# Optimization experiments

Hardware: AMD Instinct MI355X
Metric: run time of the kernel (lower is better)

Reference implementation:

```python
import jax, jax.numpy as jnp
import numpy as np


def setup_inputs() -> dict:
    key = jax.random.key(0)
    k1, k2, k3, k4 = jax.random.split(key, 4)
    B, S, K, N = 2, 1024, 4096, 4096
    x = jax.random.normal(k1, (B, S, K), dtype=jnp.float32)
    # int8 weights in [-128, 127]
    weight = jax.random.randint(k2, (N, K), -128, 128, dtype=jnp.int8)
    # per-output-channel dequant scales (small positive values)
    scales = jax.random.uniform(k3, (N,), dtype=jnp.float32, minval=0.005, maxval=0.02)
    bias = jax.random.normal(k4, (N,), dtype=jnp.float32) * 0.1
    return {"x": x, "weight": weight, "scales": scales, "bias": bias}


def reference(x, weight, scales, bias):
    # F.linear(x, weight.to(x.dtype)): [B,S,K] @ [N,K]^T -> [B,S,N]
    w = weight.astype(x.dtype)
    y = jnp.einsum('bsk,nk->bsn', x, w)
    # per-output-channel scale + bias epilogue
    return y * scales + bias
```

## Files before the change

### kernel.cpp

```cpp
#include <hip/hip_runtime.h>
#include <hip/hip_bf16.h>
#include <stdint.h>

#define M_DIM 2048
#define N_DIM 4096
#define K_DIM 4096

#define BM 128
#define BN 256
#define BK 128

#define NSLOT 3
#define ASLOT (BM * BK)
#define BSLOT (BN * BK)

#define NT (K_DIM / BK)

typedef __attribute__((ext_vector_type(4))) int   int4v;
typedef __attribute__((ext_vector_type(4))) float f32x4;

__device__ __forceinline__ void load_lds16(const void* g, void* l) {
    __builtin_amdgcn_global_load_lds(
        (const __attribute__((address_space(1))) void*)g,
        (__attribute__((address_space(3))) void*)l,
        16, 0, 0);
}

__global__ __launch_bounds__(256) void quant_x(const float* __restrict__ x,
                                               int8_t* __restrict__ Aq,
                                               float* __restrict__ sx) {
    const int row = blockIdx.x;
    const int tid = threadIdx.x;
    const float4* xr = (const float4*)(x + (size_t)row * K_DIM);

    float4 v[4];
    float mx = 0.f;
#pragma unroll
    for (int p = 0; p < 4; p++) {
        v[p] = xr[p * 256 + tid];
        mx = fmaxf(mx, fmaxf(fmaxf(fabsf(v[p].x), fabsf(v[p].y)),
                             fmaxf(fabsf(v[p].z), fabsf(v[p].w))));
    }
#pragma unroll
    for (int off = 32; off >= 1; off >>= 1)
        mx = fmaxf(mx, __shfl_xor(mx, off, 64));

    __shared__ float wmax[4];
    __shared__ float smax;
    if ((tid & 63) == 0) wmax[tid >> 6] = mx;
    __syncthreads();
    if (tid == 0) {
        float m = fmaxf(fmaxf(wmax[0], wmax[1]), fmaxf(wmax[2], wmax[3]));
        m = fmaxf(m, 1e-20f);
        smax = m;
        sx[row] = m * (1.0f / 127.0f);
    }
    __syncthreads();
    const float inv = 127.0f / smax;

    int* out = (int*)Aq + (size_t)row * (K_DIM / 4);
#pragma unroll
    for (int p = 0; p < 4; p++) {
        int q0 = (int)__builtin_rintf(v[p].x * inv);
        int q1 = (int)__builtin_rintf(v[p].y * inv);
        int q2 = (int)__builtin_rintf(v[p].z * inv);
        int q3 = (int)__builtin_rintf(v[p].w * inv);
        q0 = max(-127, min(127, q0)); q1 = max(-127, min(127, q1));
        q2 = max(-127, min(127, q2)); q3 = max(-127, min(127, q3));
        out[p * 256 + tid] = (q0 & 255) | ((q1 & 255) << 8) |
                             ((q2 & 255) << 16) | ((q3 & 255) << 24);
    }
}

__global__ __launch_bounds__(256) void cvt_w8(const int* __restrict__ w,
                                              int8_t* __restrict__ Bq) {
    size_t i = ((size_t)blockIdx.x * 256 + threadIdx.x) * 16;
    int4 a0 = *(const int4*)(w + i);
    int4 a1 = *(const int4*)(w + i + 4);
    int4 a2 = *(const int4*)(w + i + 8);
    int4 a3 = *(const int4*)(w + i + 12);
    uint4 t;
    t.x = (a0.x & 255) | ((a0.y & 255) << 8) | ((a0.z & 255) << 16) | ((a0.w & 255) << 24);
    t.y = (a1.x & 255) | ((a1.y & 255) << 8) | ((a1.z & 255) << 16) | ((a1.w & 255) << 24);
    t.z = (a2.x & 255) | ((a2.y & 255) << 8) | ((a2.z & 255) << 16) | ((a2.w & 255) << 24);
    t.w = (a3.x & 255) | ((a3.y & 255) << 8) | ((a3.z & 255) << 16) | ((a3.w & 255) << 24);
    *(uint4*)(Bq + i) = t;
}


__global__ __launch_bounds__(512, 2) void gemm_bt_i8(
    const int8_t* __restrict__ A,
    const int8_t* __restrict__ B,
    const float*  __restrict__ sx,
    const float*  __restrict__ scales,
    const float*  __restrict__ bias,
    float* __restrict__ C)
{
    __shared__ __align__(16) int8_t As[NSLOT * ASLOT];
    __shared__ __align__(16) int8_t Bs[NSLOT * BSLOT];

    const int tid  = threadIdx.x;

    const int bid   = blockIdx.x;
    const int xcd   = bid & 7;
    const int local = bid >> 3;
    const int bm    = (xcd >> 2) * 8 + (local >> 2);
    const int bn    = (xcd & 3) * 4 + (local & 3);

    const int lane = tid & 63;
    const int wave = tid >> 6;
    const int wm   = (wave >> 2) * 64;
    const int wn   = (wave & 3) * 64;
    const int l16  = lane & 15;
    const int quad = lane >> 4;
    const int swz  = l16 & 7;

    const int srow = tid >> 3;
    const int cgp  = tid & 7;
    const int cgl  = cgp ^ (srow & 7);

    const int8_t* ga = A + (size_t)(bm * BM + srow) * K_DIM + cgl * 16;
    const int8_t* gb = B + (size_t)(bn * BN + srow) * K_DIM + cgl * 16;
    const int la = tid * 16;

#define STAGE(slot, koff) do {                                               \
        load_lds16(ga + (koff),                 As + (slot) * ASLOT + la);   \
        load_lds16(ga + 64 * K_DIM + (koff),    As + (slot) * ASLOT + 8192 + la); \
        load_lds16(gb + (koff),                 Bs + (slot) * BSLOT + la);   \
        load_lds16(gb + 64 * K_DIM + (koff),    Bs + (slot) * BSLOT + 8192 + la); \
        load_lds16(gb + 128 * K_DIM + (koff),   Bs + (slot) * BSLOT + 16384 + la); \
        load_lds16(gb + 192 * K_DIM + (koff),   Bs + (slot) * BSLOT + 24576 + la); \
    } while (0)

    int4v acc[4][4] = {};

#define COMPUTE(slot) do {                                                   \
        const int8_t* Ab = As + (slot) * ASLOT;                              \
        const int8_t* Bb = Bs + (slot) * BSLOT;                              \
        _Pragma("unroll")                                                    \
        for (int h = 0; h < 2; h++) {                                        \
            const int cp = (h * 4 + quad) ^ swz;                             \
            int4v af[4], bfr[4];                                             \
            _Pragma("unroll")                                                \
            for (int i = 0; i < 4; i++)                                      \
                af[i] = *(const int4v*)(Ab + (wm + i * 16 + l16) * BK + cp * 16); \
            _Pragma("unroll")                                                \
            for (int j = 0; j < 4; j++)                                      \
                bfr[j] = *(const int4v*)(Bb + (wn + j * 16 + l16) * BK + cp * 16); \
            __builtin_amdgcn_s_setprio(1);                                   \
            _Pragma("unroll")                                                \
            for (int i = 0; i < 4; i++)                                      \
                _Pragma("unroll")                                            \
                for (int j = 0; j < 4; j++)                                  \
                    acc[i][j] = __builtin_amdgcn_mfma_i32_16x16x64_i8(       \
                        af[i], bfr[j], acc[i][j], 0, 0, 0);                  \
            __builtin_amdgcn_s_setprio(0);                                   \
        }                                                                    \
    } while (0)

    STAGE(0, 0);
    STAGE(1, BK);

    int s0 = 0, s1 = 1, s2 = 2;

    for (int t = 0; t < NT - 2; ++t) {
        asm volatile("s_waitcnt vmcnt(6)" ::: "memory");
        __builtin_amdgcn_s_barrier();
        STAGE(s2, (t + 2) * BK);
        COMPUTE(s0);
        const int tmp = s0; s0 = s1; s1 = s2; s2 = tmp;
    }

    asm volatile("s_waitcnt vmcnt(6)" ::: "memory");
    __builtin_amdgcn_s_barrier();
    COMPUTE(s0);
    { const int tmp = s0; s0 = s1; s1 = s2; s2 = tmp; }

    asm volatile("s_waitcnt vmcnt(0)" ::: "memory");
    __builtin_amdgcn_s_barrier();
    COMPUTE(s0);

#undef STAGE
#undef COMPUTE

    float sxr[16];
#pragma unroll
    for (int i = 0; i < 4; i++)
#pragma unroll
        for (int r = 0; r < 4; r++)
            sxr[i * 4 + r] = sx[bm * BM + wm + i * 16 + quad * 4 + r];

#pragma unroll
    for (int j = 0; j < 4; j++) {
        const int col = bn * BN + wn + j * 16 + l16;
        const float s = scales[col];
        const float b = bias[col];
#pragma unroll
        for (int i = 0; i < 4; i++) {
            const int row0 = bm * BM + wm + i * 16 + quad * 4;
#pragma unroll
            for (int r = 0; r < 4; r++) {
                C[(size_t)(row0 + r) * N_DIM + col] =
                    (float)acc[i][j][r] * (sxr[i * 4 + r] * s) + b;
            }
        }
    }
}


extern "C" void kernel_launch(void* const* d_in, const int* in_sizes, int n_in,
                              void* d_out, int out_size, void* d_ws, size_t ws_size,
                              hipStream_t stream) {
    const float* x      = (const float*)d_in[0];
    const int*   w      = (const int*)d_in[1];
    const float* scales = (const float*)d_in[2];
    const float* bias   = (const float*)d_in[3];
    float*       out    = (float*)d_out;

    int8_t* Aq = (int8_t*)d_ws;
    int8_t* Bq = (int8_t*)d_ws + (size_t)M_DIM * K_DIM;
    float*  sx = (float*)((int8_t*)d_ws + (size_t)(M_DIM + N_DIM) * K_DIM);

    quant_x<<<M_DIM, 256, 0, stream>>>(x, Aq, sx);
    cvt_w8<<<(int)((size_t)N_DIM * K_DIM / 16 / 256), 256, 0, stream>>>(w, Bq);

    gemm_bt_i8<<<256, 512, 0, stream>>>(Aq, Bq, sx, scales, bias, out);
}
```

Before: 175.3 us.

## Split K-tile staging across two phases with barriers and remap block tiling

Restructures the GEMM main loop so each K tile is processed in two phases. Each phase issues half of the next tile's global-to-LDS loads after its LDS fragment reads, then synchronizes with barriers around the MFMA block, aiming to interleave memory traffic with compute more evenly. It also changes the block-to-tile mapping per XCD from 8x4 to 4x8 tiles, which alters L2 reuse, and drops the min-2-blocks occupancy hint from launch bounds. The extra barriers per phase add synchronization cost, and the loop is no longer peeled.

```diff
diff --git a/kernel.cpp b/kernel.cpp
--- a/kernel.cpp
+++ b/kernel.cpp
@@ -13,7 +13,6 @@
 #define NSLOT 3
 #define ASLOT (BM * BK)
 #define BSLOT (BN * BK)
-
 #define NT (K_DIM / BK)
 
 typedef __attribute__((ext_vector_type(4))) int   int4v;
@@ -88,7 +87,7 @@
 }
 
 
-__global__ __launch_bounds__(512, 2) void gemm_bt_i8(
+__global__ __launch_bounds__(512) void gemm_bt_i8(
     const int8_t* __restrict__ A,
     const int8_t* __restrict__ B,
     const float*  __restrict__ sx,
@@ -104,8 +103,8 @@
     const int bid   = blockIdx.x;
     const int xcd   = bid & 7;
     const int local = bid >> 3;
-    const int bm    = (xcd >> 2) * 8 + (local >> 2);
-    const int bn    = (xcd & 3) * 4 + (local & 3);
+    const int bm    = (xcd >> 1) * 4 + (local >> 3);
+    const int bn    = (xcd & 1) * 8 + (local & 7);
 
     const int lane = tid & 63;
     const int wave = tid >> 6;
@@ -116,72 +115,78 @@
     const int swz  = l16 & 7;
 
     const int srow = tid >> 3;
-    const int cgp  = tid & 7;
-    const int cgl  = cgp ^ (srow & 7);
-
-    const int8_t* ga = A + (size_t)(bm * BM + srow) * K_DIM + cgl * 16;
-    const int8_t* gb = B + (size_t)(bn * BN + srow) * K_DIM + cgl * 16;
+    const int cgl  = (tid & 7) ^ (srow & 7);
+
+    const int8_t* ga0 = A + (size_t)(bm * BM + srow)       * K_DIM + cgl * 16;
+    const int8_t* ga1 = A + (size_t)(bm * BM + 64 + srow)  * K_DIM + cgl * 16;
+    const int8_t* gb0 = B + (size_t)(bn * BN + srow)       * K_DIM + cgl * 16;
+    const int8_t* gb1 = B + (size_t)(bn * BN + 64 + srow)  * K_DIM + cgl * 16;
+    const int8_t* gb2 = B + (size_t)(bn * BN + 128 + srow) * K_DIM + cgl * 16;
+    const int8_t* gb3 = B + (size_t)(bn * BN + 192 + srow) * K_DIM + cgl * 16;
     const int la = tid * 16;
 
-#define STAGE(slot, koff) do {                                               \
-        load_lds16(ga + (koff),                 As + (slot) * ASLOT + la);   \
-        load_lds16(ga + 64 * K_DIM + (koff),    As + (slot) * ASLOT + 8192 + la); \
-        load_lds16(gb + (koff),                 Bs + (slot) * BSLOT + la);   \
-        load_lds16(gb + 64 * K_DIM + (koff),    Bs + (slot) * BSLOT + 8192 + la); \
-        load_lds16(gb + 128 * K_DIM + (koff),   Bs + (slot) * BSLOT + 16384 + la); \
-        load_lds16(gb + 192 * K_DIM + (koff),   Bs + (slot) * BSLOT + 24576 + la); \
+#define STAGE1(slot, k0_) do {                                               \
+        load_lds16(ga0 + (k0_), As + (slot) * ASLOT + la);                   \
+        load_lds16(ga1 + (k0_), As + (slot) * ASLOT + 8192 + la);            \
+        load_lds16(gb0 + (k0_), Bs + (slot) * BSLOT + la);                   \
     } while (0)
+#define STAGE2(slot, k0_) do {                                               \
+        load_lds16(gb1 + (k0_), Bs + (slot) * BSLOT + 8192 + la);            \
+        load_lds16(gb2 + (k0_), Bs + (slot) * BSLOT + 16384 + la);           \
+        load_lds16(gb3 + (k0_), Bs + (slot) * BSLOT + 24576 + la);           \
+    } while (0)
 
     int4v acc[4][4] = {};
 
-#define COMPUTE(slot) do {                                                   \
-        const int8_t* Ab = As + (slot) * ASLOT;                              \
-        const int8_t* Bb = Bs + (slot) * BSLOT;                              \
+#define PHASE(h_, Ab, Bb, STG, VMW) do {                                     \
+        const int cp_ = ((h_) * 4 + quad) ^ swz;                             \
+        int4v af[4], bf[4];                                                  \
         _Pragma("unroll")                                                    \
-        for (int h = 0; h < 2; h++) {                                        \
-            const int cp = (h * 4 + quad) ^ swz;                             \
-            int4v af[4], bfr[4];                                             \
+        for (int i = 0; i < 4; i++)                                          \
+            af[i] = *(const int4v*)((Ab) + (wm + i * 16 + l16) * BK + cp_ * 16); \
+        _Pragma("unroll")                                                    \
+        for (int j = 0; j < 4; j++)                                          \
+            bf[j] = *(const int4v*)((Bb) + (wn + j * 16 + l16) * BK + cp_ * 16); \
+        STG;                                                                 \
+        VMW;                                                                 \
+        __builtin_amdgcn_s_barrier();                                        \
+        asm volatile("s_waitcnt lgkmcnt(0)" ::: "memory");                   \
+        __builtin_amdgcn_s_setprio(1);                                       \
+        _Pragma("unroll")                                                    \
+        for (int j = 0; j < 4; j++)                                          \
             _Pragma("unroll")                                                \
             for (int i = 0; i < 4; i++)                                      \
-                af[i] = *(const int4v*)(Ab + (wm + i * 16 + l16) * BK + cp * 16); \
-            _Pragma("unroll")                                                \
-            for (int j = 0; j < 4; j++)                                      \
-                bfr[j] = *(const int4v*)(Bb + (wn + j * 16 + l16) * BK + cp * 16); \
-            __builtin_amdgcn_s_setprio(1);                                   \
-            _Pragma("unroll")                                                \
-            for (int i = 0; i < 4; i++)                                      \
-                _Pragma("unroll")                                            \
-                for (int j = 0; j < 4; j++)                                  \
-                    acc[i][j] = __builtin_amdgcn_mfma_i32_16x16x64_i8(       \
-                        af[i], bfr[j], acc[i][j], 0, 0, 0);                  \
-            __builtin_amdgcn_s_setprio(0);                                   \
-        }                                                                    \
+                acc[i][j] = __builtin_amdgcn_mfma_i32_16x16x64_i8(           \
+                    af[i], bf[j], acc[i][j], 0, 0, 0);                       \
+        __builtin_amdgcn_s_setprio(0);                                       \
+        __builtin_amdgcn_s_barrier();                                        \
     } while (0)
 
-    STAGE(0, 0);
-    STAGE(1, BK);
-
-    int s0 = 0, s1 = 1, s2 = 2;
-
-    for (int t = 0; t < NT - 2; ++t) {
-        asm volatile("s_waitcnt vmcnt(6)" ::: "memory");
-        __builtin_amdgcn_s_barrier();
-        STAGE(s2, (t + 2) * BK);
-        COMPUTE(s0);
-        const int tmp = s0; s0 = s1; s1 = s2; s2 = tmp;
-    }
-
+    STAGE1(0, 0);      STAGE2(0, 0);
+    STAGE1(1, BK);     STAGE2(1, BK);
     asm volatile("s_waitcnt vmcnt(6)" ::: "memory");
     __builtin_amdgcn_s_barrier();
-    COMPUTE(s0);
-    { const int tmp = s0; s0 = s1; s1 = s2; s2 = tmp; }
-
-    asm volatile("s_waitcnt vmcnt(0)" ::: "memory");
-    __builtin_amdgcn_s_barrier();
-    COMPUTE(s0);
-
-#undef STAGE
-#undef COMPUTE
+
+    int s0 = 0, s1 = 1, s2 = 2;
+    for (int t = 0; t < NT; ++t) {
+        const int8_t* Ab = As + s0 * ASLOT;
+        const int8_t* Bb = Bs + s0 * BSLOT;
+        const int kf = (t + 2) * BK;
+        if (t + 2 < NT) {
+            PHASE(0, Ab, Bb, STAGE1(s2, kf), (void)0);
+            PHASE(1, Ab, Bb, STAGE2(s2, kf),
+                  asm volatile("s_waitcnt vmcnt(6)" ::: "memory"));
+        } else {
+            PHASE(0, Ab, Bb, (void)0, (void)0);
+            PHASE(1, Ab, Bb, (void)0,
+                  asm volatile("s_waitcnt vmcnt(0)" ::: "memory"));
+        }
+        const int tmp = s0; s0 = s1; s1 = s2; s2 = tmp;
+    }
+
+#undef PHASE
+#undef STAGE1
+#undef STAGE2
 
     float sxr[16];
 #pragma unroll
```

Result: faster. 169.4 us (-3.4%).

## Shrink GEMM tiles to 128x128x64 with new LDS swizzle and 2D grid

Applied to the files above, without the earlier changes.

Reduces the int8 GEMM block tile from 128x256x128 to 128x128x64. This quadruples the LDS-per-stage savings, doubles the grid to 512 blocks and raises launch bounds to allow four blocks per CU. The LDS layout and swizzle are rewritten so each 64-byte K row maps to packed 128-byte lines. The XCD-aware block remapping and the setprio hints are dropped in favour of a plain 2D grid. Smaller tiles improve occupancy and load balance but lower arithmetic intensity per LDS byte and increase global traffic for A and B.

```diff
diff --git a/kernel.cpp b/kernel.cpp
--- a/kernel.cpp
+++ b/kernel.cpp
@@ -7,13 +7,12 @@
 #define K_DIM 4096
 
 #define BM 128
-#define BN 256
-#define BK 128
+#define BN 128
+#define BK 64
 
 #define NSLOT 3
 #define ASLOT (BM * BK)
 #define BSLOT (BN * BK)
-
 #define NT (K_DIM / BK)
 
 typedef __attribute__((ext_vector_type(4))) int   int4v;
@@ -88,7 +87,7 @@
 }
 
 
-__global__ __launch_bounds__(512, 2) void gemm_bt_i8(
+__global__ __launch_bounds__(512, 4) void gemm_bt_i8(
     const int8_t* __restrict__ A,
     const int8_t* __restrict__ B,
     const float*  __restrict__ sx,
@@ -100,82 +99,65 @@
     __shared__ __align__(16) int8_t Bs[NSLOT * BSLOT];
 
     const int tid  = threadIdx.x;
-
-    const int bid   = blockIdx.x;
-    const int xcd   = bid & 7;
-    const int local = bid >> 3;
-    const int bm    = (xcd >> 2) * 8 + (local >> 2);
-    const int bn    = (xcd & 3) * 4 + (local & 3);
-
+    const int bm   = blockIdx.y;
+    const int bn   = blockIdx.x;
     const int lane = tid & 63;
     const int wave = tid >> 6;
     const int wm   = (wave >> 2) * 64;
-    const int wn   = (wave & 3) * 64;
+    const int wn   = (wave & 3) * 32;
     const int l16  = lane & 15;
     const int quad = lane >> 4;
-    const int swz  = l16 & 7;
-
-    const int srow = tid >> 3;
-    const int cgp  = tid & 7;
-    const int cgl  = cgp ^ (srow & 7);
-
-    const int8_t* ga = A + (size_t)(bm * BM + srow) * K_DIM + cgl * 16;
-    const int8_t* gb = B + (size_t)(bn * BN + srow) * K_DIM + cgl * 16;
+
+    const int e    = (tid & 7) ^ ((tid >> 3) & 7);
+    const int arow = 2 * (tid >> 3) + (e >> 2);
+    const int acol = (e & 3) * 16;
+
+    const int8_t* ga = A + (size_t)(bm * BM + arow) * K_DIM + acol;
+    const int8_t* gb = B + (size_t)(bn * BN + arow) * K_DIM + acol;
     const int la = tid * 16;
 
-#define STAGE(slot, koff) do {                                               \
-        load_lds16(ga + (koff),                 As + (slot) * ASLOT + la);   \
-        load_lds16(ga + 64 * K_DIM + (koff),    As + (slot) * ASLOT + 8192 + la); \
-        load_lds16(gb + (koff),                 Bs + (slot) * BSLOT + la);   \
-        load_lds16(gb + 64 * K_DIM + (koff),    Bs + (slot) * BSLOT + 8192 + la); \
-        load_lds16(gb + 128 * K_DIM + (koff),   Bs + (slot) * BSLOT + 16384 + la); \
-        load_lds16(gb + 192 * K_DIM + (koff),   Bs + (slot) * BSLOT + 24576 + la); \
+#define STAGE(slot, k0_) do {                                    \
+        load_lds16(ga + (k0_), As + (slot) * ASLOT + la);        \
+        load_lds16(gb + (k0_), Bs + (slot) * BSLOT + la);        \
     } while (0)
 
-    int4v acc[4][4] = {};
-
-#define COMPUTE(slot) do {                                                   \
-        const int8_t* Ab = As + (slot) * ASLOT;                              \
-        const int8_t* Bb = Bs + (slot) * BSLOT;                              \
+    const int lslot = (((l16 & 1) << 2) | quad) ^ (l16 >> 1);
+    const int lpart = (l16 >> 1) * 128 + lslot * 16;
+    const int abase = wm * 64 + lpart;
+    const int bbase = wn * 64 + lpart;
+
+    int4v acc[4][2] = {};
+
+#define COMPUTE(s_) do {                                                     \
+        const int8_t* Ab = As + (s_) * ASLOT;                                \
+        const int8_t* Bb = Bs + (s_) * BSLOT;                                \
+        int4v af[4], bf[2];                                                  \
         _Pragma("unroll")                                                    \
-        for (int h = 0; h < 2; h++) {                                        \
-            const int cp = (h * 4 + quad) ^ swz;                             \
-            int4v af[4], bfr[4];                                             \
+        for (int i = 0; i < 4; i++)                                          \
+            af[i] = *(const int4v*)(Ab + abase + i * 1024);                  \
+        _Pragma("unroll")                                                    \
+        for (int j = 0; j < 2; j++)                                          \
+            bf[j] = *(const int4v*)(Bb + bbase + j * 1024);                  \
+        _Pragma("unroll")                                                    \
+        for (int i = 0; i < 4; i++)                                          \
             _Pragma("unroll")                                                \
-            for (int i = 0; i < 4; i++)                                      \
-                af[i] = *(const int4v*)(Ab + (wm + i * 16 + l16) * BK + cp * 16); \
-            _Pragma("unroll")                                                \
-            for (int j = 0; j < 4; j++)                                      \
-                bfr[j] = *(const int4v*)(Bb + (wn + j * 16 + l16) * BK + cp * 16); \
-            __builtin_amdgcn_s_setprio(1);                                   \
-            _Pragma("unroll")                                                \
-            for (int i = 0; i < 4; i++)                                      \
-                _Pragma("unroll")                                            \
-                for (int j = 0; j < 4; j++)                                  \
-                    acc[i][j] = __builtin_amdgcn_mfma_i32_16x16x64_i8(       \
-                        af[i], bfr[j], acc[i][j], 0, 0, 0);                  \
-            __builtin_amdgcn_s_setprio(0);                                   \
-        }                                                                    \
+            for (int j = 0; j < 2; j++)                                      \
+                acc[i][j] = __builtin_amdgcn_mfma_i32_16x16x64_i8(           \
+                    af[i], bf[j], acc[i][j], 0, 0, 0);                       \
     } while (0)
 
     STAGE(0, 0);
     STAGE(1, BK);
 
     int s0 = 0, s1 = 1, s2 = 2;
-
-    for (int t = 0; t < NT - 2; ++t) {
-        asm volatile("s_waitcnt vmcnt(6)" ::: "memory");
+    for (int t = 0; t < NT - 1; ++t) {
+        asm volatile("s_waitcnt vmcnt(2)" ::: "memory");
         __builtin_amdgcn_s_barrier();
-        STAGE(s2, (t + 2) * BK);
+        if (t + 2 < NT)
+            STAGE(s2, (t + 2) * BK);
         COMPUTE(s0);
         const int tmp = s0; s0 = s1; s1 = s2; s2 = tmp;
     }
-
-    asm volatile("s_waitcnt vmcnt(6)" ::: "memory");
-    __builtin_amdgcn_s_barrier();
-    COMPUTE(s0);
-    { const int tmp = s0; s0 = s1; s1 = s2; s2 = tmp; }
-
     asm volatile("s_waitcnt vmcnt(0)" ::: "memory");
     __builtin_amdgcn_s_barrier();
     COMPUTE(s0);
@@ -191,7 +173,7 @@
             sxr[i * 4 + r] = sx[bm * BM + wm + i * 16 + quad * 4 + r];
 
 #pragma unroll
-    for (int j = 0; j < 4; j++) {
+    for (int j = 0; j < 2; j++) {
         const int col = bn * BN + wn + j * 16 + l16;
         const float s = scales[col];
         const float b = bias[col];
@@ -224,5 +206,6 @@
     quant_x<<<M_DIM, 256, 0, stream>>>(x, Aq, sx);
     cvt_w8<<<(int)((size_t)N_DIM * K_DIM / 16 / 256), 256, 0, stream>>>(w, Bq);
 
-    gemm_bt_i8<<<256, 512, 0, stream>>>(Aq, Bq, sx, scales, bias, out);
-}
+    dim3 grid(N_DIM / BN, M_DIM / BM);
+    gemm_bt_i8<<<grid, 512, 0, stream>>>(Aq, Bq, sx, scales, bias, out);
+}
```

New measurement: 176.5 us. About the same (+0.7%).
